# Kernel optimization log

Hardware: AMD Instinct MI355X
Metric: run time of the kernel (lower is better)

Reference implementation:

```python
import jax, jax.numpy as jnp
import numpy as np

HID = 128
K = 8
G = 1024        # number of graphs (jets)
N_SV = 16       # secondary vertices per graph
N_TRK = 64      # tracks per graph


def _mlp2(x, W1, b1, W2, b2):
    # Linear -> ELU -> Linear -> ReLU (the sv/trk encoders)
    h = jax.nn.elu(x @ W1 + b1)
    return jax.nn.relu(h @ W2 + b2)


def _dynamic_edge_conv(src, dst, W, b, k):
    # DynamicEdgeConv with bipartite input (x_src, x_dst):
    #   edge_index = knn(src, dst, k) per graph (Euclidean in feature space)
    #   message    = nn(cat([x_i, x_j - x_i]))  with x_i = dst(target), x_j = src(neighbor)
    #   aggr       = max over the k neighbors of each target
    # src: [G, Ns, D], dst: [G, Nq, D]
    dots = jnp.einsum('gqd,gsd->gqs', dst, src)
    d2 = (jnp.sum(dst * dst, -1)[:, :, None] - 2.0 * dots
          + jnp.sum(src * src, -1)[:, None, :])            # [G, Nq, Ns]
    _, idx = jax.lax.top_k(-d2, k)                          # k nearest sources, [G, Nq, k]
    xj = jax.vmap(lambda s, i: s[i])(src, idx)              # gather neighbors [G, Nq, k, D]
    xi = dst[:, :, None, :]                                 # [G, Nq, 1, D]
    edge_feat = jnp.concatenate([jnp.broadcast_to(xi, xj.shape), xj - xi], axis=-1)
    msg = jax.nn.elu(edge_feat @ W + b)                     # [G, Nq, k, D]
    return jnp.max(msg, axis=2)                             # max-scatter -> [G, Nq, D]


def setup_inputs() -> dict:
    key = jax.random.key(0)
    ks = jax.random.split(key, 16)
    s = 0.05
    inp = {
        'x_sv': jax.random.normal(ks[0], (G * N_SV, 2), jnp.float32),
        'x_trk': jax.random.normal(ks[1], (G * N_TRK, 8), jnp.float32),
        # sv encoder
        'W_sv1': jax.random.normal(ks[2], (2, HID), jnp.float32) * s,
        'b_sv1': jnp.zeros((HID,), jnp.float32),
        'W_sv2': jax.random.normal(ks[3], (HID, HID), jnp.float32) * s,
        'b_sv2': jnp.zeros((HID,), jnp.float32),
        # trk encoder
        'W_trk1': jax.random.normal(ks[4], (8, HID), jnp.float32) * s,
        'b_trk1': jnp.zeros((HID,), jnp.float32),
        'W_trk2': jax.random.normal(ks[5], (HID, HID), jnp.float32) * s,
        'b_trk2': jnp.zeros((HID,), jnp.float32),
        # edge-conv MLPs (Linear(2*HID, HID) + ELU)
        'W_c1': jax.random.normal(ks[6], (2 * HID, HID), jnp.float32) * s,
        'b_c1': jnp.zeros((HID,), jnp.float32),
        'W_c2': jax.random.normal(ks[7], (2 * HID, HID), jnp.float32) * s,
        'b_c2': jnp.zeros((HID,), jnp.float32),
        # output head 128->64->32->4->1
        'W_o1': jax.random.normal(ks[8], (HID, 64), jnp.float32) * s,
        'b_o1': jnp.zeros((64,), jnp.float32),
        'W_o2': jax.random.normal(ks[9], (64, 32), jnp.float32) * s,
        'b_o2': jnp.zeros((32,), jnp.float32),
        'W_o3': jax.random.normal(ks[10], (32, 4), jnp.float32) * s,
        'b_o3': jnp.zeros((4,), jnp.float32),
        'W_o4': jax.random.normal(ks[11], (4, 1), jnp.float32) * s,
        'b_o4': jnp.zeros((1,), jnp.float32),
        # block-structured batch assignment (sorted, equal-size graphs)
        'batch_sv': jnp.arange(G * N_SV, dtype=jnp.int64 if jax.config.jax_enable_x64 else jnp.int32) // N_SV,
        'batch_trk': jnp.arange(G * N_TRK, dtype=jnp.int64 if jax.config.jax_enable_x64 else jnp.int32) // N_TRK,
    }
    return inp


def reference(x_sv, x_trk, W_sv1, b_sv1, W_sv2, b_sv2, W_trk1, b_trk1, W_trk2, b_trk2,
              W_c1, b_c1, W_c2, b_c2, W_o1, b_o1, W_o2, b_o2, W_o3, b_o3, W_o4, b_o4,
              batch_sv, batch_trk):
    # Batches are equal-size contiguous blocks (see setup_inputs), so per-graph
    # knn/gather/max are expressed as batched ops over a leading G dimension.
    sv = _mlp2(x_sv, W_sv1, b_sv1, W_sv2, b_sv2).reshape(G, N_SV, HID)
    trk = _mlp2(x_trk, W_trk1, b_trk1, W_trk2, b_trk2).reshape(G, N_TRK, HID)
    # conv_1: sources = encoded SVs, targets = encoded tracks
    f1 = _dynamic_edge_conv(sv, trk, W_c1, b_c1, K)          # [G, N_TRK, HID]
    # conv_2: sources = f1 (per-track), targets = encoded tracks
    f2 = _dynamic_edge_conv(f1, trk, W_c2, b_c2, K)          # [G, N_TRK, HID]
    # avg_pool_x with cluster == batch: mean over tracks of each graph
    pooled = jnp.mean(f2, axis=1)                            # [G, HID]
    h = jax.nn.elu(pooled @ W_o1 + b_o1)
    h = jax.nn.elu(h @ W_o2 + b_o2)
    h = jax.nn.elu(h @ W_o3 + b_o3)
    out = h @ W_o4 + b_o4                                    # [G, 1]
    batch = jnp.arange(G)
    return out, batch
```

## Files before the change

kernel.cpp:

```cpp
#include <hip/hip_runtime.h>

#define G_    1024
#define TPB   512
#define INF_F 3.4e38f

typedef __attribute__((ext_vector_type(8))) short short8;
typedef __attribute__((ext_vector_type(4))) float f32x4;

__device__ __forceinline__ float elu_fast(float x) { return x > 0.f ? x : __expf(x) - 1.f; }
__device__ __forceinline__ float elu_ref(float x)  { return x > 0.f ? x : expm1f(x); }

#define RB(r, c)     ((r)*128 + (((c) + 8*(r)) & 127))

#define FMA4(acc_, sc_, wv_) do { (acc_).x = fmaf((sc_),(wv_).x,(acc_).x); \
                                  (acc_).y = fmaf((sc_),(wv_).y,(acc_).y); \
                                  (acc_).z = fmaf((sc_),(wv_).z,(acc_).z); \
                                  (acc_).w = fmaf((sc_),(wv_).w,(acc_).w); } while(0)
#define MAX4(mm_, bb_)       do { (mm_).x = fmaxf((mm_).x,(bb_).x); \
                                  (mm_).y = fmaxf((mm_).y,(bb_).y); \
                                  (mm_).z = fmaxf((mm_).z,(bb_).z); \
                                  (mm_).w = fmaxf((mm_).w,(bb_).w); } while(0)

#define MFMA1(acc_, A_, B_) \
    acc_ = __builtin_amdgcn_mfma_f32_16x16x32_bf16((A_), (B_), (acc_), 0, 0, 0)

__device__ __forceinline__ unsigned short bf16_of(float v) {
    unsigned u = __float_as_uint(v);
    u = u + 0x7FFFu + ((u >> 16) & 1u);
    return (unsigned short)(u >> 16);
}
__device__ __forceinline__ float f32_of(unsigned short h) {
    return __uint_as_float((unsigned)h << 16);
}

__global__ void prep_pack(const float* __restrict__ Wtrk2, const float* __restrict__ Wsv2,
                          const float* __restrict__ Wc1,   const float* __restrict__ Wc2,
                          unsigned short* __restrict__ wsu) {
    const int o = blockIdx.x * 256 + threadIdx.x;
    if (o >= 6 * 16384) return;
    const int m = o >> 14, pos = o & 16383;
    const int j = pos & 7, lane = (pos >> 3) & 63, tile = pos >> 9;
    const int ks = tile >> 3, ni = tile & 7;
    const int d = ks * 32 + (lane >> 4) * 8 + j;
    const int c = ni * 16 + (lane & 15);
    const int e = d * 128 + c;
    float v;
    switch (m) {
        case 0: v = Wtrk2[e]; break;
        case 1: v = Wsv2[e]; break;
        case 2: v = Wc1[16384 + e]; break;
        case 3: v = Wc1[e] - Wc1[16384 + e]; break;
        case 4: v = Wc2[e] - Wc2[16384 + e]; break;
        default: v = Wc2[16384 + e]; break;
    }
    wsu[m * 16384 + pos] = bf16_of(v);
}

#define LOADB1(B_, m_, pos_) B_ = *(const short8*)(wsu + (m_) * 16384 + (pos_))
#define LDFRAG(buf_, r_, k0_) (*(const short8*)&(buf_)[RB((r_), (k0_))])

__global__ __launch_bounds__(TPB, 8)
void fused_mfma(const float* __restrict__ x_sv,  const float* __restrict__ x_trk,
                const float* __restrict__ W_sv1, const float* __restrict__ b_sv1,
                const float* __restrict__ b_sv2,
                const float* __restrict__ W_trk1,const float* __restrict__ b_trk1,
                const float* __restrict__ b_trk2,
                const float* __restrict__ b_c1,  const float* __restrict__ b_c2,
                const float* __restrict__ W_o1,  const float* __restrict__ b_o1,
                const float* __restrict__ W_o2,  const float* __restrict__ b_o2,
                const float* __restrict__ W_o3,  const float* __restrict__ b_o3,
                const float* __restrict__ W_o4,  const float* __restrict__ b_o4,
                const unsigned short* __restrict__ wsu,
                float* __restrict__ out)
{
    __shared__ __align__(16) char sAraw[16384];
    __shared__ __align__(16) char sBraw[16384];
    __shared__ __align__(16) char sCraw[8192];
    short*    sAh = (short*)sAraw;    float* sAf = (float*)sAraw;
    short*    sBh = (short*)sBraw;    float* sBf = (float*)sBraw;
    unsigned* sBu = (unsigned*)sBraw;
    short*    sCh = (short*)sCraw;    float* sCf = (float*)sCraw;
    unsigned* sCu = (unsigned*)sCraw;

    const int g    = blockIdx.x;
    const int tid  = threadIdx.x;
    const int c128 = tid & 127;
    const int g4   = tid >> 7;
    const int wv   = tid >> 6;
    const int lane = tid & 63;
    const int quad = lane >> 4;
    const int ln   = lane & 15;

    sCf[tid] = x_trk[(size_t)g * 512 + tid];
    if (tid < 32) sCf[512 + tid] = x_sv[(size_t)g * 32 + tid];
    __syncthreads();

    {
        float w[8];
        #pragma unroll
        for (int k = 0; k < 8; k++) w[k] = W_trk1[k * 128 + c128];
        const float b1 = b_trk1[c128];
        #pragma unroll
        for (int i = 0; i < 16; i++) {
            const int r = g4 * 16 + i;
            float xr[8];
            *(float4*)&xr[0] = *(const float4*)&sCf[r * 8];
            *(float4*)&xr[4] = *(const float4*)&sCf[r * 8 + 4];
            float acc = b1;
            #pragma unroll
            for (int k = 0; k < 8; k++) acc = fmaf(xr[k], w[k], acc);
            sBh[RB(r, c128)] = bf16_of(elu_fast(acc));
        }
    }
    __syncthreads();

    {
        const int mi = wv >> 1, nb = (wv & 1) * 4;
        const int row = mi * 16 + ln;
        f32x4 acc[4];
        #pragma unroll
        for (int t = 0; t < 4; t++) {
            const float bz = b_trk2[(nb + t) * 16 + ln];
            acc[t] = (f32x4){bz, bz, bz, bz};
        }
        #pragma unroll 2
        for (int ks = 0; ks < 4; ks++) {
            const int k0 = ks * 32 + quad * 8;
            const short8 A = LDFRAG(sBh, row, k0);
            #pragma unroll
            for (int t = 0; t < 4; t++) {
                const int pos = ((ks * 8 + (nb + t)) * 64 + lane) * 8;
                short8 B;
                LOADB1(B, 0, pos);
                MFMA1(acc[t], A, B);
            }
        }
        #pragma unroll
        for (int t = 0; t < 4; t++)
            #pragma unroll
            for (int r = 0; r < 4; r++)
                sAh[RB(mi * 16 + quad * 4 + r, (nb + t) * 16 + ln)] =
                    bf16_of(fmaxf(acc[t][r], 0.f));
    }
    __syncthreads();

    {
        const float w0 = W_sv1[c128], w1 = W_sv1[128 + c128];
        const float b1 = b_sv1[c128];
        #pragma unroll
        for (int i = 0; i < 4; i++) {
            const int s = g4 * 4 + i;
            sBh[RB(s, c128)] = bf16_of(
                elu_fast(fmaf(sCf[512 + s * 2 + 1], w1, fmaf(sCf[512 + s * 2], w0, b1))));
        }
    }
    __syncthreads();

    {
        const int ni = wv;
        const float bz = b_sv2[ni * 16 + ln];
        f32x4 acc = (f32x4){bz, bz, bz, bz};
        #pragma unroll 2
        for (int ks = 0; ks < 4; ks++) {
            const int k0 = ks * 32 + quad * 8;
            const short8 A = LDFRAG(sBh, ln, k0);
            const int pos = ((ks * 8 + ni) * 64 + lane) * 8;
            short8 B;
            LOADB1(B, 1, pos);
            MFMA1(acc, A, B);
        }
        #pragma unroll
        for (int r = 0; r < 4; r++) {
            const float v = fmaxf(acc[r], 0.f);
            sCh[RB(quad * 4 + r, ni * 16 + ln)] = bf16_of(v);
            float p = v * v;
            #pragma unroll
            for (int o = 1; o <= 8; o <<= 1) p += __shfl_xor(p, o, 16);
            if (ln == 0) sBf[2048 + ni * 16 + quad * 4 + r] = p;
        }
    }
    __syncthreads();

    {
        const int ni = wv;
        const bool doP4 = (wv < 4);
        f32x4 accB = (f32x4){0.f, 0.f, 0.f, 0.f};
        f32x4 accS = (f32x4){0.f, 0.f, 0.f, 0.f};
        #pragma unroll 2
        for (int ks = 0; ks < 4; ks++) {
            const int k0 = ks * 32 + quad * 8;
            const short8 S = LDFRAG(sCh, ln, k0);
            const int pos = ((ks * 8 + ni) * 64 + lane) * 8;
            short8 B;
            LOADB1(B, 2, pos);
            MFMA1(accB, S, B);
            if (doP4) {
                const short8 T = LDFRAG(sAh, wv * 16 + ln, k0);
                MFMA1(accS, T, S);
            }
        }
        float nsv = 0.f;
        if (doP4) {
            #pragma unroll
            for (int p = 0; p < 8; p++) nsv += sBf[2048 + p * 16 + ln];
        }
        __syncthreads();
        #pragma unroll
        for (int r = 0; r < 4; r++)
            sCf[(quad * 4 + r) * 128 + ni * 16 + ln] = accB[r];
        if (doP4) {
            #pragma unroll
            for (int r = 0; r < 4; r++)
                sBf[(wv * 16 + quad * 4 + r) * 17 + ln] = fmaf(-2.f, accS[r], nsv);
        }
    }
    __syncthreads();

    {
        const int q  = tid >> 3;
        const int s0 = tid & 7;
        float sc0 = sBf[q * 17 + s0];
        float sc1 = sBf[q * 17 + s0 + 8];
        unsigned pack1 = 0u;
        #pragma unroll
        for (int r = 0; r < 8; r++) {
            float bv = sc0; int bs = s0;
            if (sc1 < bv) { bv = sc1; bs = s0 + 8; }
            #pragma unroll
            for (int o = 1; o <= 4; o <<= 1) {
                const float ov = __shfl_xor(bv, o, 8);
                const int   os = __shfl_xor(bs, o, 8);
                if (ov < bv || (ov == bv && os < bs)) { bv = ov; bs = os; }
            }
            pack1 |= (unsigned)bs << (4 * r);
            if (bs == s0)     sc0 = INF_F;
            if (bs == s0 + 8) sc1 = INF_F;
        }
        if (s0 == 0) sBu[1088 + q] = pack1;
    }
    __syncthreads();

    {
        const int mi = wv >> 1, nb = (wv & 1) * 4;
        const int row = mi * 16 + ln;
        f32x4 a1acc[4];
        #pragma unroll
        for (int t = 0; t < 4; t++) {
            const float bz1 = b_c1[(nb + t) * 16 + ln];
            a1acc[t] = (f32x4){bz1, bz1, bz1, bz1};
        }
        #pragma unroll 2
        for (int ks = 0; ks < 4; ks++) {
            const int k0 = ks * 32 + quad * 8;
            const short8 A = LDFRAG(sAh, row, k0);
            #pragma unroll
            for (int t = 0; t < 4; t++) {
                const int pos = ((ks * 8 + (nb + t)) * 64 + lane) * 8;
                short8 B;
                LOADB1(B, 3, pos);
                MFMA1(a1acc[t], A, B);
            }
        }
        unsigned pk[4];
        #pragma unroll
        for (int r = 0; r < 4; r++) pk[r] = sBu[1088 + mi * 16 + quad * 4 + r];
        __syncthreads();
        float np[4] = {0.f, 0.f, 0.f, 0.f};
        const int ccb = nb * 16 + ln;
        const float* b1base = &sCf[ccb];
        #pragma unroll
        for (int r = 0; r < 4; r++) {
            float mx0 = -INF_F, mx1 = -INF_F, mx2 = -INF_F, mx3 = -INF_F;
            #pragma unroll
            for (int j = 0; j < 8; j++) {
                const int s = (int)((pk[r] >> (4 * j)) & 15u);
                const float* rp = b1base + s * 128;
                mx0 = fmaxf(mx0, rp[0]);
                mx1 = fmaxf(mx1, rp[16]);
                mx2 = fmaxf(mx2, rp[32]);
                mx3 = fmaxf(mx3, rp[48]);
            }
            const float mxa[4] = {mx0, mx1, mx2, mx3};
            #pragma unroll
            for (int t = 0; t < 4; t++) {
                const float f = elu_fast(a1acc[t][r] + mxa[t]);
                sBh[RB(mi * 16 + quad * 4 + r, ccb + 16 * t)] = bf16_of(f);
                np[r] = fmaf(f, f, np[r]);
            }
        }
        #pragma unroll
        for (int r = 0; r < 4; r++) {
            #pragma unroll
            for (int o = 1; o <= 8; o <<= 1) np[r] += __shfl_xor(np[r], o, 16);
        }
        __syncthreads();
        if (ln == 0) {
            #pragma unroll
            for (int r = 0; r < 4; r++)
                sCf[(wv & 1) * 64 + mi * 16 + quad * 4 + r] = np[r];
        }
    }

    unsigned a2p[8];
    {
        const int mi = wv >> 1, nb = (wv & 1) * 4;
        const int row = mi * 16 + ln;
        f32x4 a2acc[4];
        #pragma unroll
        for (int t = 0; t < 4; t++) {
            const float bz2 = b_c2[(nb + t) * 16 + ln];
            a2acc[t] = (f32x4){bz2, bz2, bz2, bz2};
        }
        #pragma unroll 2
        for (int ks = 0; ks < 4; ks++) {
            const int k0 = ks * 32 + quad * 8;
            const short8 A = LDFRAG(sAh, row, k0);
            #pragma unroll
            for (int t = 0; t < 4; t++) {
                const int pos = ((ks * 8 + (nb + t)) * 64 + lane) * 8;
                short8 B;
                LOADB1(B, 4, pos);
                MFMA1(a2acc[t], A, B);
            }
        }
        #pragma unroll
        for (int t = 0; t < 4; t++) {
            a2p[2 * t]     = (unsigned)bf16_of(a2acc[t][0]) |
                             ((unsigned)bf16_of(a2acc[t][1]) << 16);
            a2p[2 * t + 1] = (unsigned)bf16_of(a2acc[t][2]) |
                             ((unsigned)bf16_of(a2acc[t][3]) << 16);
        }
    }
    __syncthreads();

    {
        const int mi = wv >> 1, nia = (wv & 1) * 2;
        const int row = mi * 16 + ln;
        float ns[2];
        #pragma unroll
        for (int u = 0; u < 2; u++) {
            const int s = (nia + u) * 16 + ln;
            ns[u] = sCf[s] + sCf[64 + s];
        }
        f32x4 acc[2];
        acc[0] = (f32x4){0.f, 0.f, 0.f, 0.f};
        acc[1] = (f32x4){0.f, 0.f, 0.f, 0.f};
        #pragma unroll 2
        for (int ks = 0; ks < 4; ks++) {
            const int k0 = ks * 32 + quad * 8;
            const short8 A = LDFRAG(sAh, row, k0);
            #pragma unroll
            for (int u = 0; u < 2; u++) {
                const short8 Bf = LDFRAG(sBh, (nia + u) * 16 + ln, k0);
                MFMA1(acc[u], A, Bf);
            }
        }
        __syncthreads();
        #pragma unroll
        for (int u = 0; u < 2; u++) {
            const int s = (nia + u) * 16 + ln;
            #pragma unroll
            for (int r = 0; r < 4; r++)
                sAf[(mi * 16 + quad * 4 + r) * 64 + s] = fmaf(-2.f, acc[u][r], ns[u]);
        }
    }
    __syncthreads();

    {
        const int q = tid >> 3;
        const int j = tid & 7;
        float v[8];
        *(float4*)&v[0] = *(const float4*)&sAf[q * 64 + 8 * j];
        *(float4*)&v[4] = *(const float4*)&sAf[q * 64 + 8 * j + 4];
        unsigned lo2 = 0u, hi2 = 0u;
        #pragma unroll
        for (int r = 0; r < 8; r++) {
            float bv = v[0]; int bs = 8 * j;
            #pragma unroll
            for (int t = 1; t < 8; t++)
                if (v[t] < bv) { bv = v[t]; bs = 8 * j + t; }
            #pragma unroll
            for (int o = 1; o <= 4; o <<= 1) {
                const float ov = __shfl_xor(bv, o, 8);
                const int   os = __shfl_xor(bs, o, 8);
                if (ov < bv || (ov == bv && os < bs)) { bv = ov; bs = os; }
            }
            if (r < 4) lo2 |= (unsigned)bs << (8 * r);
            else       hi2 |= (unsigned)bs << (8 * (r - 4));
            #pragma unroll
            for (int t = 0; t < 8; t++)
                if (bs == 8 * j + t) v[t] = INF_F;
        }
        if (j == 0) {
            sCu[128 + 2 * q]     = lo2;
            sCu[128 + 2 * q + 1] = hi2;
        }
    }
    __syncthreads();

    {
        const int mi = wv >> 1, nb = (wv & 1) * 4;
        const int row = mi * 16 + ln;
        f32x4 acc[4];
        #pragma unroll
        for (int t = 0; t < 4; t++) acc[t] = (f32x4){0.f, 0.f, 0.f, 0.f};
        #pragma unroll 2
        for (int ks = 0; ks < 4; ks++) {
            const int k0 = ks * 32 + quad * 8;
            const short8 A = LDFRAG(sBh, row, k0);
            #pragma unroll
            for (int t = 0; t < 4; t++) {
                const int pos = ((ks * 8 + (nb + t)) * 64 + lane) * 8;
                short8 B;
                LOADB1(B, 5, pos);
                MFMA1(acc[t], A, B);
            }
        }
        __syncthreads();
        float* bp = (mi < 2) ? sAf : sBf;
        const int ccb = nb * 16 + ln;
        #pragma unroll
        for (int t = 0; t < 4; t++)
            #pragma unroll
            for (int r = 0; r < 4; r++) {
                const int rr = mi * 16 + quad * 4 + r;
                bp[(rr & 31) * 128 + ccb + 16 * t] = acc[t][r];
            }
    }
    __syncthreads();

    {
        const int mi = wv >> 1, nb = (wv & 1) * 4;
        float ps[4] = {0.f, 0.f, 0.f, 0.f};
        const int ccb = nb * 16 + ln;
        const float* bA = &sAf[ccb];
        const float* bB = &sBf[ccb];
        #pragma unroll
        for (int r = 0; r < 4; r++) {
            const int rr = mi * 16 + quad * 4 + r;
            const unsigned plo = sCu[128 + 2 * rr];
            const unsigned phi = sCu[128 + 2 * rr + 1];
            float mx0 = -INF_F, mx1 = -INF_F, mx2 = -INF_F, mx3 = -INF_F;
            #pragma unroll
            for (int j = 0; j < 8; j++) {
                const int s = (int)(((j < 4) ? (plo >> (8 * j))
                                             : (phi >> (8 * (j - 4)))) & 63u);
                const float* rp = ((s < 32) ? bA : bB) + (s & 31) * 128;
                mx0 = fmaxf(mx0, rp[0]);
                mx1 = fmaxf(mx1, rp[16]);
                mx2 = fmaxf(mx2, rp[32]);
                mx3 = fmaxf(mx3, rp[48]);
            }
            const float mxa[4] = {mx0, mx1, mx2, mx3};
            #pragma unroll
            for (int t = 0; t < 4; t++) {
                const unsigned u = a2p[2 * t + (r >> 1)];
                const float a2v = __uint_as_float((r & 1) ? (u & 0xFFFF0000u) : (u << 16));
                ps[t] += elu_fast(a2v + mxa[t]);
            }
        }
        #pragma unroll
        for (int t = 0; t < 4; t++) {
            ps[t] += __shfl_xor(ps[t], 16, 64);
            ps[t] += __shfl_xor(ps[t], 32, 64);
        }
        __syncthreads();
        if (lane < 16)
            #pragma unroll
            for (int t = 0; t < 4; t++)
                sBf[mi * 128 + (nb + t) * 16 + lane] = ps[t];
    }
    __syncthreads();

    if (tid < 128) {
        const float p = (sBf[tid] + sBf[128 + tid] + sBf[256 + tid] + sBf[384 + tid]) * (1.f / 64.f);
        sBf[512 + tid] = p;
    }
    __syncthreads();
    if (tid < 64) {
        float acc = b_o1[tid];
        for (int d = 0; d < 128; d++) acc = fmaf(sBf[512 + d], W_o1[d * 64 + tid], acc);
        sBf[640 + tid] = elu_fast(acc);
    }
    __syncthreads();
    if (tid < 32) {
        float acc = b_o2[tid];
        for (int d = 0; d < 64; d++) acc = fmaf(sBf[640 + d], W_o2[d * 32 + tid], acc);
        sBf[704 + tid] = elu_fast(acc);
    }
    __syncthreads();
    if (tid < 4) {
        float acc = b_o3[tid];
        for (int d = 0; d < 32; d++) acc = fmaf(sBf[704 + d], W_o3[d * 4 + tid], acc);
        sBf[736 + tid] = elu_fast(acc);
    }
    __syncthreads();
    if (tid == 0) {
        float acc = b_o4[0];
        #pragma unroll
        for (int d = 0; d < 4; d++) acc = fmaf(sBf[736 + d], W_o4[d], acc);
        out[g] = acc;
        out[G_ + g] = (float)g;
    }
}

#define ROTV(r, d)    ((r)*128 + (((d) + 4*(r)) & 127))
#define BS1V(s, c)    (2048 + (s)*128 + (((c) + 4*(s)) & 127))
__global__ __launch_bounds__(TPB, 2)
void fused_vec(const float* __restrict__ x_sv,  const float* __restrict__ x_trk,
               const float* __restrict__ W_sv1, const float* __restrict__ b_sv1,
               const float* __restrict__ W_sv2, const float* __restrict__ b_sv2,
               const float* __restrict__ W_trk1,const float* __restrict__ b_trk1,
               const float* __restrict__ W_trk2,const float* __restrict__ b_trk2,
               const float* __restrict__ W_c1,  const float* __restrict__ b_c1,
               const float* __restrict__ W_c2,  const float* __restrict__ b_c2,
               const float* __restrict__ W_o1,  const float* __restrict__ b_o1,
               const float* __restrict__ W_o2,  const float* __restrict__ b_o2,
               const float* __restrict__ W_o3,  const float* __restrict__ b_o3,
               const float* __restrict__ W_o4,  const float* __restrict__ b_o4,
               float* __restrict__ out)
{
    __shared__ float sA[8192];
    __shared__ float sB[8192];
    __shared__ float sC[4096];
    const int g    = blockIdx.x;
    const int tid  = threadIdx.x;
    const int c128 = tid & 127;
    const int g4   = tid >> 7;
    const int cq   = tid & 31;
    const int c0   = cq * 4;
    const int rg   = tid >> 5;
    const int lane_hi = tid & 32;

    sC[2048 + tid] = x_trk[(size_t)g * 512 + tid];
    if (tid < 32) sC[2560 + tid] = x_sv[(size_t)g * 32 + tid];
    __syncthreads();
    {
        float w[8];
        #pragma unroll
        for (int k = 0; k < 8; k++) w[k] = W_trk1[k * 128 + c128];
        const float b1 = b_trk1[c128];
        #pragma unroll
        for (int i = 0; i < 16; i++) {
            const int r = g4 * 16 + i;
            float acc = b1;
            #pragma unroll
            for (int k = 0; k < 8; k++) acc = fmaf(sC[2048 + r * 8 + k], w[k], acc);
            sB[r * 128 + c128] = elu_ref(acc);
        }
    }
    __syncthreads();
    {
        const int r0 = rg * 4;
        float4 acc[4];
        const float4 bz = *(const float4*)&b_trk2[c0];
        #pragma unroll
        for (int i = 0; i < 4; i++) acc[i] = bz;
        for (int d0 = 0; d0 < 128; d0 += 4) {
            const float4 w0 = *(const float4*)&W_trk2[(d0 + 0) * 128 + c0];
            const float4 w1 = *(const float4*)&W_trk2[(d0 + 1) * 128 + c0];
            const float4 w2 = *(const float4*)&W_trk2[(d0 + 2) * 128 + c0];
            const float4 w3 = *(const float4*)&W_trk2[(d0 + 3) * 128 + c0];
            #pragma unroll
            for (int i = 0; i < 4; i++) {
                const float4 h = *(const float4*)&sB[(r0 + i) * 128 + d0];
                FMA4(acc[i], h.x, w0); FMA4(acc[i], h.y, w1);
                FMA4(acc[i], h.z, w2); FMA4(acc[i], h.w, w3);
            }
        }
        #pragma unroll
        for (int i = 0; i < 4; i++) {
            float4 r;
            r.x = fmaxf(acc[i].x, 0.f); r.y = fmaxf(acc[i].y, 0.f);
            r.z = fmaxf(acc[i].z, 0.f); r.w = fmaxf(acc[i].w, 0.f);
            *(float4*)&sA[ROTV(r0 + i, c0)] = r;
        }
    }
    __syncthreads();
    {
        const float w0 = W_sv1[c128], w1 = W_sv1[128 + c128];
        const float b1 = b_sv1[c128];
        #pragma unroll
        for (int i = 0; i < 4; i++) {
            const int s = g4 * 4 + i;
            sB[s * 128 + c128] =
                elu_ref(fmaf(sC[2560 + s * 2 + 1], w1, fmaf(sC[2560 + s * 2], w0, b1)));
        }
    }
    __syncthreads();
    {
        const int s = rg;
        float4 acc = *(const float4*)&b_sv2[c0];
        for (int d0 = 0; d0 < 128; d0 += 4) {
            const float4 w0 = *(const float4*)&W_sv2[(d0 + 0) * 128 + c0];
            const float4 w1 = *(const float4*)&W_sv2[(d0 + 1) * 128 + c0];
            const float4 w2 = *(const float4*)&W_sv2[(d0 + 2) * 128 + c0];
            const float4 w3 = *(const float4*)&W_sv2[(d0 + 3) * 128 + c0];
            const float4 h = *(const float4*)&sB[s * 128 + d0];
            FMA4(acc, h.x, w0); FMA4(acc, h.y, w1);
            FMA4(acc, h.z, w2); FMA4(acc, h.w, w3);
        }
        float4 r;
        r.x = fmaxf(acc.x, 0.f); r.y = fmaxf(acc.y, 0.f);
        r.z = fmaxf(acc.z, 0.f); r.w = fmaxf(acc.w, 0.f);
        *(float4*)&sC[ROTV(s, c0)] = r;
    }
    __syncthreads();
    unsigned pack1;
    {
        {
            const int s = rg;
            float4 acc = {0.f, 0.f, 0.f, 0.f};
            for (int d0 = 0; d0 < 128; d0 += 4) {
                const float4 e  = *(const float4*)&sC[ROTV(s, d0)];
                const float4 w0 = *(const float4*)&W_c1[(128 + d0 + 0) * 128 + c0];
                const float4 w1 = *(const float4*)&W_c1[(128 + d0 + 1) * 128 + c0];
                const float4 w2 = *(const float4*)&W_c1[(128 + d0 + 2) * 128 + c0];
                const float4 w3 = *(const float4*)&W_c1[(128 + d0 + 3) * 128 + c0];
                FMA4(acc, e.x, w0); FMA4(acc, e.y, w1);
                FMA4(acc, e.z, w2); FMA4(acc, e.w, w3);
            }
            *(float4*)&sC[BS1V(s, c0)] = acc;
        }
        const int q  = tid >> 3;
        const int s0 = tid & 7;
        float d0a = 0.f, d1a = 0.f, n0 = 0.f, n1 = 0.f;
        for (int d0 = 0; d0 < 128; d0 += 4) {
            const float4 t  = *(const float4*)&sA[ROTV(q, d0)];
            const float4 v0 = *(const float4*)&sC[ROTV(s0, d0)];
            const float4 v1 = *(const float4*)&sC[ROTV(s0 + 8, d0)];
            d0a += t.x * v0.x + t.y * v0.y + t.z * v0.z + t.w * v0.w;
            d1a += t.x * v1.x + t.y * v1.y + t.z * v1.z + t.w * v1.w;
            n0  += v0.x * v0.x + v0.y * v0.y + v0.z * v0.z + v0.w * v0.w;
            n1  += v1.x * v1.x + v1.y * v1.y + v1.z * v1.z + v1.w * v1.w;
        }
        float sc0 = fmaf(-2.f, d0a, n0);
        float sc1 = fmaf(-2.f, d1a, n1);
        pack1 = 0u;
        #pragma unroll
        for (int r = 0; r < 8; r++) {
            float bv = sc0; int bs = s0;
            if (sc1 < bv) { bv = sc1; bs = s0 + 8; }
            #pragma unroll
            for (int o = 1; o <= 4; o <<= 1) {
                const float ov = __shfl_xor(bv, o, 8);
                const int   os = __shfl_xor(bs, o, 8);
                if (ov < bv || (ov == bv && os < bs)) { bv = ov; bs = os; }
            }
            pack1 |= (unsigned)bs << (4 * r);
            if (bs == s0)     sc0 = INF_F;
            if (bs == s0 + 8) sc1 = INF_F;
        }
    }
    __syncthreads();
    float4 a2v[4];
    {
        const int q0 = rg * 4;
        float4 a1[4];
        const float4 bc1 = *(const float4*)&b_c1[c0];
        const float4 bc2 = *(const float4*)&b_c2[c0];
        #pragma unroll
        for (int i = 0; i < 4; i++) { a1[i] = bc1; a2v[i] = bc2; }
        for (int d0 = 0; d0 < 128; d0 += 4) {
            float4 t[4];
            #pragma unroll
            for (int i = 0; i < 4; i++) t[i] = *(const float4*)&sA[ROTV(q0 + i, d0)];
            #pragma unroll
            for (int dj = 0; dj < 4; dj++) {
                float4 wv;
                const float4 wa = *(const float4*)&W_c1[(d0 + dj) * 128 + c0];
                const float4 wb = *(const float4*)&W_c1[(128 + d0 + dj) * 128 + c0];
                wv.x = wa.x - wb.x; wv.y = wa.y - wb.y;
                wv.z = wa.z - wb.z; wv.w = wa.w - wb.w;
                FMA4(a1[0], ((const float*)&t[0])[dj], wv);
                FMA4(a1[1], ((const float*)&t[1])[dj], wv);
                FMA4(a1[2], ((const float*)&t[2])[dj], wv);
                FMA4(a1[3], ((const float*)&t[3])[dj], wv);
            }
            #pragma unroll
            for (int dj = 0; dj < 4; dj++) {
                float4 wv;
                const float4 wa = *(const float4*)&W_c2[(d0 + dj) * 128 + c0];
                const float4 wb = *(const float4*)&W_c2[(128 + d0 + dj) * 128 + c0];
                wv.x = wa.x - wb.x; wv.y = wa.y - wb.y;
                wv.z = wa.z - wb.z; wv.w = wa.w - wb.w;
                FMA4(a2v[0], ((const float*)&t[0])[dj], wv);
                FMA4(a2v[1], ((const float*)&t[1])[dj], wv);
                FMA4(a2v[2], ((const float*)&t[2])[dj], wv);
                FMA4(a2v[3], ((const float*)&t[3])[dj], wv);
            }
        }
        #pragma unroll
        for (int i = 0; i < 4; i++) {
            const int q = q0 + i;
            const unsigned pk = __shfl(pack1, 8 * i + lane_hi);
            float4 m = {-INF_F, -INF_F, -INF_F, -INF_F};
            #pragma unroll
            for (int j = 0; j < 8; j++) {
                const int s = (int)((pk >> (4 * j)) & 15u);
                const float4 b = *(const float4*)&sC[BS1V(s, c0)];
                MAX4(m, b);
            }
            float4 f;
            f.x = elu_ref(a1[i].x + m.x); f.y = elu_ref(a1[i].y + m.y);
            f.z = elu_ref(a1[i].z + m.z); f.w = elu_ref(a1[i].w + m.w);
            *(float4*)&sB[ROTV(q, c0)] = f;
        }
    }
    __syncthreads();
    {
        const int s  = tid & 63;
        const int q0 = (tid >> 6) * 8;
        float acc[8];
        #pragma unroll
        for (int i = 0; i < 8; i++) acc[i] = 0.f;
        float nrm = 0.f;
        for (int d0 = 0; d0 < 128; d0 += 4) {
            const float4 f = *(const float4*)&sB[ROTV(s, d0)];
            nrm = fmaf(f.x, f.x, nrm); nrm = fmaf(f.y, f.y, nrm);
            nrm = fmaf(f.z, f.z, nrm); nrm = fmaf(f.w, f.w, nrm);
            #pragma unroll
            for (int i = 0; i < 8; i++) {
                const float4 t = *(const float4*)&sA[ROTV(q0 + i, d0)];
                acc[i] = fmaf(t.x, f.x, acc[i]); acc[i] = fmaf(t.y, f.y, acc[i]);
                acc[i] = fmaf(t.z, f.z, acc[i]); acc[i] = fmaf(t.w, f.w, acc[i]);
            }
        }
        #pragma unroll
        for (int i = 0; i < 8; i++)
            sC[(q0 + i) * 64 + s] = fmaf(-2.f, acc[i], nrm);
    }
    __syncthreads();
    unsigned lo2, hi2;
    {
        const int q = tid >> 3;
        const int j = tid & 7;
        float v[8];
        *(float4*)&v[0] = *(const float4*)&sC[q * 64 + 8 * j];
        *(float4*)&v[4] = *(const float4*)&sC[q * 64 + 8 * j + 4];
        lo2 = 0u; hi2 = 0u;
        #pragma unroll
        for (int r = 0; r < 8; r++) {
            float bv = v[0]; int bs = 8 * j;
            #pragma unroll
            for (int t = 1; t < 8; t++)
                if (v[t] < bv) { bv = v[t]; bs = 8 * j + t; }
            #pragma unroll
            for (int o = 1; o <= 4; o <<= 1) {
                const float ov = __shfl_xor(bv, o, 8);
                const int   os = __shfl_xor(bs, o, 8);
                if (ov < bv || (ov == bv && os < bs)) { bv = ov; bs = os; }
            }
            if (r < 4) lo2 |= (unsigned)bs << (8 * r);
            else       hi2 |= (unsigned)bs << (8 * (r - 4));
            #pragma unroll
            for (int t = 0; t < 8; t++)
                if (bs == 8 * j + t) v[t] = INF_F;
        }
        const int r0 = rg * 4;
        float4 acc[4];
        #pragma unroll
        for (int i = 0; i < 4; i++) acc[i] = make_float4(0.f, 0.f, 0.f, 0.f);
        for (int d0 = 0; d0 < 128; d0 += 4) {
            const float4 w0 = *(const float4*)&W_c2[(128 + d0 + 0) * 128 + c0];
            const float4 w1 = *(const float4*)&W_c2[(128 + d0 + 1) * 128 + c0];
            const float4 w2 = *(const float4*)&W_c2[(128 + d0 + 2) * 128 + c0];
            const float4 w3 = *(const float4*)&W_c2[(128 + d0 + 3) * 128 + c0];
            #pragma unroll
            for (int i = 0; i < 4; i++) {
                const float4 f = *(const float4*)&sB[ROTV(r0 + i, d0)];
                FMA4(acc[i], f.x, w0); FMA4(acc[i], f.y, w1);
                FMA4(acc[i], f.z, w2); FMA4(acc[i], f.w, w3);
            }
        }
        #pragma unroll
        for (int i = 0; i < 4; i++)
            *(float4*)&sA[ROTV(r0 + i, c0)] = acc[i];
    }
    __syncthreads();
    {
        const int q0 = rg * 4;
        float4 ps = {0.f, 0.f, 0.f, 0.f};
        #pragma unroll
        for (int i = 0; i < 4; i++) {
            const unsigned plo = __shfl(lo2, 8 * i + lane_hi);
            const unsigned phi = __shfl(hi2, 8 * i + lane_hi);
            float4 m = {-INF_F, -INF_F, -INF_F, -INF_F};
            #pragma unroll
            for (int j = 0; j < 8; j++) {
                const int s = (int)(((j < 4) ? (plo >> (8 * j)) : (phi >> (8 * (j - 4)))) & 63u);
                const float4 b = *(const float4*)&sA[ROTV(s, c0)];
                MAX4(m, b);
            }
            ps.x += elu_ref(a2v[i].x + m.x); ps.y += elu_ref(a2v[i].y + m.y);
            ps.z += elu_ref(a2v[i].z + m.z); ps.w += elu_ref(a2v[i].w + m.w);
        }
        *(float4*)&sB[rg * 128 + c0] = ps;
    }
    __syncthreads();
    if (tid < 128) {
        float p = 0.f;
        #pragma unroll
        for (int t = 0; t < 16; t++) p += sB[t * 128 + tid];
        sB[2048 + tid] = p * (1.f / 64.f);
    }
    __syncthreads();
    if (tid < 64) {
        float acc = b_o1[tid];
        for (int d = 0; d < 128; d++) acc = fmaf(sB[2048 + d], W_o1[d * 64 + tid], acc);
        sB[2176 + tid] = elu_ref(acc);
    }
    __syncthreads();
    if (tid < 32) {
        float acc = b_o2[tid];
        for (int d = 0; d < 64; d++) acc = fmaf(sB[2176 + d], W_o2[d * 32 + tid], acc);
        sB[2240 + tid] = elu_ref(acc);
    }
    __syncthreads();
    if (tid < 4) {
        float acc = b_o3[tid];
        for (int d = 0; d < 32; d++) acc = fmaf(sB[2240 + d], W_o3[d * 4 + tid], acc);
        sB[2272 + tid] = elu_ref(acc);
    }
    __syncthreads();
    if (tid == 0) {
        float acc = b_o4[0];
        #pragma unroll
        for (int d = 0; d < 4; d++) acc = fmaf(sB[2272 + d], W_o4[d], acc);
        out[g] = acc;
        out[G_ + g] = (float)g;
    }
}

extern "C" void kernel_launch(void* const* d_in, const int* in_sizes, int n_in,
                              void* d_out, int out_size, void* d_ws, size_t ws_size,
                              hipStream_t stream) {
    const float* x_sv   = (const float*)d_in[0];
    const float* x_trk  = (const float*)d_in[1];
    const float* W_sv1  = (const float*)d_in[2];
    const float* b_sv1  = (const float*)d_in[3];
    const float* W_sv2  = (const float*)d_in[4];
    const float* b_sv2  = (const float*)d_in[5];
    const float* W_trk1 = (const float*)d_in[6];
    const float* b_trk1 = (const float*)d_in[7];
    const float* W_trk2 = (const float*)d_in[8];
    const float* b_trk2 = (const float*)d_in[9];
    const float* W_c1   = (const float*)d_in[10];
    const float* b_c1   = (const float*)d_in[11];
    const float* W_c2   = (const float*)d_in[12];
    const float* b_c2   = (const float*)d_in[13];
    const float* W_o1   = (const float*)d_in[14];
    const float* b_o1   = (const float*)d_in[15];
    const float* W_o2   = (const float*)d_in[16];
    const float* b_o2   = (const float*)d_in[17];
    const float* W_o3   = (const float*)d_in[18];
    const float* b_o3   = (const float*)d_in[19];
    const float* W_o4   = (const float*)d_in[20];
    const float* b_o4   = (const float*)d_in[21];
    float* out = (float*)d_out;

    const size_t WS_NEED = (size_t)6 * 16384 * sizeof(unsigned short);
    if (ws_size >= WS_NEED && d_ws != nullptr) {
        unsigned short* wsu = (unsigned short*)d_ws;
        prep_pack<<<384, 256, 0, stream>>>(W_trk2, W_sv2, W_c1, W_c2, wsu);
        fused_mfma<<<G_, TPB, 0, stream>>>(x_sv, x_trk, W_sv1, b_sv1, b_sv2,
                                           W_trk1, b_trk1, b_trk2, b_c1, b_c2,
                                           W_o1, b_o1, W_o2, b_o2, W_o3, b_o3,
                                           W_o4, b_o4, wsu, out);
    } else {
        fused_vec<<<G_, TPB, 0, stream>>>(x_sv, x_trk, W_sv1, b_sv1, W_sv2, b_sv2,
                                          W_trk1, b_trk1, W_trk2, b_trk2,
                                          W_c1, b_c1, W_c2, b_c2,
                                          W_o1, b_o1, W_o2, b_o2, W_o3, b_o3,
                                          W_o4, b_o4, out);
    }
}
```

Baseline: 167.9 us.

## Restructure MFMA stages to cut live accumulators and remap final gather per column

```diff
diff --git a/kernel.cpp b/kernel.cpp
--- a/kernel.cpp
+++ b/kernel.cpp
@@ -31,6 +31,9 @@
 }
 __device__ __forceinline__ float f32_of(unsigned short h) {
     return __uint_as_float((unsigned)h << 16);
+}
+__device__ __forceinline__ unsigned packbf2(float a, float b) {
+    return (unsigned)bf16_of(a) | ((unsigned)bf16_of(b) << 16);
 }
 
 __global__ void prep_pack(const float* __restrict__ Wtrk2, const float* __restrict__ Wsv2,
@@ -80,7 +83,6 @@
     short*    sBh = (short*)sBraw;    float* sBf = (float*)sBraw;
     unsigned* sBu = (unsigned*)sBraw;
     short*    sCh = (short*)sCraw;    float* sCf = (float*)sCraw;
-    unsigned* sCu = (unsigned*)sCraw;
 
     const int g    = blockIdx.x;
     const int tid  = threadIdx.x;
@@ -115,32 +117,28 @@
     __syncthreads();
 
     {
-        const int mi = wv >> 1, nb = (wv & 1) * 4;
-        const int row = mi * 16 + ln;
-        f32x4 acc[4];
-        #pragma unroll
-        for (int t = 0; t < 4; t++) {
-            const float bz = b_trk2[(nb + t) * 16 + ln];
-            acc[t] = (f32x4){bz, bz, bz, bz};
-        }
-        #pragma unroll 2
-        for (int ks = 0; ks < 4; ks++) {
-            const int k0 = ks * 32 + quad * 8;
-            const short8 A = LDFRAG(sBh, row, k0);
-            #pragma unroll
-            for (int t = 0; t < 4; t++) {
-                const int pos = ((ks * 8 + (nb + t)) * 64 + lane) * 8;
+        const int cb = wv * 16 + ln;
+        const float bz = b_trk2[cb];
+        #pragma unroll 1
+        for (int half = 0; half < 2; half++) {
+            f32x4 a0 = (f32x4){bz, bz, bz, bz};
+            f32x4 a1 = (f32x4){bz, bz, bz, bz};
+            #pragma unroll 2
+            for (int ks = 0; ks < 4; ks++) {
+                const int k0 = ks * 32 + quad * 8;
+                const short8 A0 = LDFRAG(sBh, half * 32 + ln, k0);
+                const short8 A1 = LDFRAG(sBh, half * 32 + 16 + ln, k0);
                 short8 B;
-                LOADB1(B, 0, pos);
-                MFMA1(acc[t], A, B);
-            }
-        }
-        #pragma unroll
-        for (int t = 0; t < 4; t++)
-            #pragma unroll
-            for (int r = 0; r < 4; r++)
-                sAh[RB(mi * 16 + quad * 4 + r, (nb + t) * 16 + ln)] =
-                    bf16_of(fmaxf(acc[t][r], 0.f));
+                LOADB1(B, 0, ((ks * 8 + wv) * 64 + lane) * 8);
+                MFMA1(a0, A0, B);
+                MFMA1(a1, A1, B);
+            }
+            #pragma unroll
+            for (int r = 0; r < 4; r++) {
+                sAh[RB(half * 32 + quad * 4 + r, cb)]      = bf16_of(fmaxf(a0[r], 0.f));
+                sAh[RB(half * 32 + 16 + quad * 4 + r, cb)] = bf16_of(fmaxf(a1[r], 0.f));
+            }
+        }
     }
     __syncthreads();
 
@@ -164,9 +162,8 @@
         for (int ks = 0; ks < 4; ks++) {
             const int k0 = ks * 32 + quad * 8;
             const short8 A = LDFRAG(sBh, ln, k0);
-            const int pos = ((ks * 8 + ni) * 64 + lane) * 8;
             short8 B;
-            LOADB1(B, 1, pos);
+            LOADB1(B, 1, ((ks * 8 + ni) * 64 + lane) * 8);
             MFMA1(acc, A, B);
         }
         #pragma unroll
@@ -190,9 +187,8 @@
         for (int ks = 0; ks < 4; ks++) {
             const int k0 = ks * 32 + quad * 8;
             const short8 S = LDFRAG(sCh, ln, k0);
-            const int pos = ((ks * 8 + ni) * 64 + lane) * 8;
             short8 B;
-            LOADB1(B, 2, pos);
+            LOADB1(B, 2, ((ks * 8 + ni) * 64 + lane) * 8);
             MFMA1(accB, S, B);
             if (doP4) {
                 const short8 T = LDFRAG(sAh, wv * 16 + ln, k0);
@@ -243,49 +239,47 @@
     {
         const int mi = wv >> 1, nb = (wv & 1) * 4;
         const int row = mi * 16 + ln;
-        f32x4 a1acc[4];
-        #pragma unroll
-        for (int t = 0; t < 4; t++) {
-            const float bz1 = b_c1[(nb + t) * 16 + ln];
-            a1acc[t] = (f32x4){bz1, bz1, bz1, bz1};
-        }
-        #pragma unroll 2
-        for (int ks = 0; ks < 4; ks++) {
-            const int k0 = ks * 32 + quad * 8;
-            const short8 A = LDFRAG(sAh, row, k0);
-            #pragma unroll
-            for (int t = 0; t < 4; t++) {
-                const int pos = ((ks * 8 + (nb + t)) * 64 + lane) * 8;
-                short8 B;
-                LOADB1(B, 3, pos);
-                MFMA1(a1acc[t], A, B);
-            }
-        }
+        const int ccb = nb * 16 + ln;
         unsigned pk[4];
         #pragma unroll
         for (int r = 0; r < 4; r++) pk[r] = sBu[1088 + mi * 16 + quad * 4 + r];
-        __syncthreads();
         float np[4] = {0.f, 0.f, 0.f, 0.f};
-        const int ccb = nb * 16 + ln;
-        const float* b1base = &sCf[ccb];
-        #pragma unroll
-        for (int r = 0; r < 4; r++) {
-            float mx0 = -INF_F, mx1 = -INF_F, mx2 = -INF_F, mx3 = -INF_F;
-            #pragma unroll
-            for (int j = 0; j < 8; j++) {
-                const int s = (int)((pk[r] >> (4 * j)) & 15u);
-                const float* rp = b1base + s * 128;
-                mx0 = fmaxf(mx0, rp[0]);
-                mx1 = fmaxf(mx1, rp[16]);
-                mx2 = fmaxf(mx2, rp[32]);
-                mx3 = fmaxf(mx3, rp[48]);
-            }
-            const float mxa[4] = {mx0, mx1, mx2, mx3};
-            #pragma unroll
-            for (int t = 0; t < 4; t++) {
-                const float f = elu_fast(a1acc[t][r] + mxa[t]);
-                sBh[RB(mi * 16 + quad * 4 + r, ccb + 16 * t)] = bf16_of(f);
-                np[r] = fmaf(f, f, np[r]);
+        #pragma unroll 1
+        for (int half = 0; half < 2; half++) {
+            f32x4 a0, a1c;
+            {
+                const float bz0 = b_c1[(nb + half * 2) * 16 + ln];
+                const float bz1 = b_c1[(nb + half * 2 + 1) * 16 + ln];
+                a0  = (f32x4){bz0, bz0, bz0, bz0};
+                a1c = (f32x4){bz1, bz1, bz1, bz1};
+            }
+            #pragma unroll 2
+            for (int ks = 0; ks < 4; ks++) {
+                const int k0 = ks * 32 + quad * 8;
+                const short8 A = LDFRAG(sAh, row, k0);
+                short8 B0, B1;
+                LOADB1(B0, 3, ((ks * 8 + nb + half * 2) * 64 + lane) * 8);
+                LOADB1(B1, 3, ((ks * 8 + nb + half * 2 + 1) * 64 + lane) * 8);
+                MFMA1(a0, A, B0);
+                MFMA1(a1c, A, B1);
+            }
+            if (half == 0) __syncthreads();
+            #pragma unroll
+            for (int r = 0; r < 4; r++) {
+                float mx0 = -INF_F, mx1 = -INF_F;
+                #pragma unroll
+                for (int j = 0; j < 8; j++) {
+                    const int s = (int)((pk[r] >> (4 * j)) & 15u);
+                    const float* rp = &sCf[s * 128 + ccb + half * 32];
+                    mx0 = fmaxf(mx0, rp[0]);
+                    mx1 = fmaxf(mx1, rp[16]);
+                }
+                const float f0 = elu_fast(a0[r] + mx0);
+                const float f1v = elu_fast(a1c[r] + mx1);
+                sBh[RB(mi * 16 + quad * 4 + r, ccb + half * 32)]      = bf16_of(f0);
+                sBh[RB(mi * 16 + quad * 4 + r, ccb + half * 32 + 16)] = bf16_of(f1v);
+                np[r] = fmaf(f0, f0, np[r]);
+                np[r] = fmaf(f1v, f1v, np[r]);
             }
         }
         #pragma unroll
@@ -303,32 +297,26 @@
 
     unsigned a2p[8];
     {
-        const int mi = wv >> 1, nb = (wv & 1) * 4;
-        const int row = mi * 16 + ln;
-        f32x4 a2acc[4];
-        #pragma unroll
-        for (int t = 0; t < 4; t++) {
-            const float bz2 = b_c2[(nb + t) * 16 + ln];
-            a2acc[t] = (f32x4){bz2, bz2, bz2, bz2};
-        }
-        #pragma unroll 2
-        for (int ks = 0; ks < 4; ks++) {
-            const int k0 = ks * 32 + quad * 8;
-            const short8 A = LDFRAG(sAh, row, k0);
-            #pragma unroll
-            for (int t = 0; t < 4; t++) {
-                const int pos = ((ks * 8 + (nb + t)) * 64 + lane) * 8;
+        const int cb = wv * 16 + ln;
+        const float bz2 = b_c2[cb];
+        #pragma unroll 1
+        for (int half = 0; half < 2; half++) {
+            f32x4 a0 = (f32x4){bz2, bz2, bz2, bz2};
+            f32x4 a1 = (f32x4){bz2, bz2, bz2, bz2};
+            #pragma unroll 2
+            for (int ks = 0; ks < 4; ks++) {
+                const int k0 = ks * 32 + quad * 8;
+                const short8 A0 = LDFRAG(sAh, half * 32 + ln, k0);
+                const short8 A1 = LDFRAG(sAh, half * 32 + 16 + ln, k0);
                 short8 B;
-                LOADB1(B, 4, pos);
-                MFMA1(a2acc[t], A, B);
-            }
-        }
-        #pragma unroll
-        for (int t = 0; t < 4; t++) {
-            a2p[2 * t]     = (unsigned)bf16_of(a2acc[t][0]) |
-                             ((unsigned)bf16_of(a2acc[t][1]) << 16);
-            a2p[2 * t + 1] = (unsigned)bf16_of(a2acc[t][2]) |
-                             ((unsigned)bf16_of(a2acc[t][3]) << 16);
+                LOADB1(B, 4, ((ks * 8 + wv) * 64 + lane) * 8);
+                MFMA1(a0, A0, B);
+                MFMA1(a1, A1, B);
+            }
+            a2p[half * 4 + 0] = packbf2(a0[0], a0[1]);
+            a2p[half * 4 + 1] = packbf2(a0[2], a0[3]);
+            a2p[half * 4 + 2] = packbf2(a1[0], a1[1]);
+            a2p[half * 4 + 3] = packbf2(a1[2], a1[3]);
         }
     }
     __syncthreads();
@@ -366,13 +354,14 @@
     }
     __syncthreads();
 
+    unsigned lo2, hi2;
     {
         const int q = tid >> 3;
         const int j = tid & 7;
         float v[8];
         *(float4*)&v[0] = *(const float4*)&sAf[q * 64 + 8 * j];
         *(float4*)&v[4] = *(const float4*)&sAf[q * 64 + 8 * j + 4];
-        unsigned lo2 = 0u, hi2 = 0u;
+        lo2 = 0u; hi2 = 0u;
         #pragma unroll
         for (int r = 0; r < 8; r++) {
             float bv = v[0]; int bs = 8 * j;
@@ -391,114 +380,118 @@
             for (int t = 0; t < 8; t++)
                 if (bs == 8 * j + t) v[t] = INF_F;
         }
-        if (j == 0) {
-            sCu[128 + 2 * q]     = lo2;
-            sCu[128 + 2 * q + 1] = hi2;
-        }
-    }
-    __syncthreads();
-
-    {
-        const int mi = wv >> 1, nb = (wv & 1) * 4;
-        const int row = mi * 16 + ln;
-        f32x4 acc[4];
-        #pragma unroll
-        for (int t = 0; t < 4; t++) acc[t] = (f32x4){0.f, 0.f, 0.f, 0.f};
+    }
+    __syncthreads();
+
+    {
+        const int cb = wv * 16 + ln;
+        {
+            f32x4 a0 = (f32x4){0.f, 0.f, 0.f, 0.f};
+            f32x4 a1 = (f32x4){0.f, 0.f, 0.f, 0.f};
+            #pragma unroll 2
+            for (int ks = 0; ks < 4; ks++) {
+                const int k0 = ks * 32 + quad * 8;
+                const short8 A0 = LDFRAG(sBh, ln, k0);
+                const short8 A1 = LDFRAG(sBh, 16 + ln, k0);
+                short8 B;
+                LOADB1(B, 5, ((ks * 8 + wv) * 64 + lane) * 8);
+                MFMA1(a0, A0, B);
+                MFMA1(a1, A1, B);
+            }
+            #pragma unroll
+            for (int r = 0; r < 4; r++) {
+                sAf[(quad * 4 + r) * 128 + cb]        = a0[r];
+                sAf[(16 + quad * 4 + r) * 128 + cb]   = a1[r];
+            }
+        }
+        {
+            f32x4 a = (f32x4){0.f, 0.f, 0.f, 0.f};
+            #pragma unroll 2
+            for (int ks = 0; ks < 4; ks++) {
+                const int k0 = ks * 32 + quad * 8;
+                const short8 A = LDFRAG(sBh, 32 + ln, k0);
+                short8 B;
+                LOADB1(B, 5, ((ks * 8 + wv) * 64 + lane) * 8);
+                MFMA1(a, A, B);
+            }
+            #pragma unroll
+            for (int r = 0; r < 4; r++)
+                sCf[(quad * 4 + r) * 128 + cb] = a[r];
+        }
+        f32x4 c = (f32x4){0.f, 0.f, 0.f, 0.f};
         #pragma unroll 2
         for (int ks = 0; ks < 4; ks++) {
             const int k0 = ks * 32 + quad * 8;
-            const short8 A = LDFRAG(sBh, row, k0);
-            #pragma unroll
-            for (int t = 0; t < 4; t++) {
-                const int pos = ((ks * 8 + (nb + t)) * 64 + lane) * 8;
-                short8 B;
-                LOADB1(B, 5, pos);
-                MFMA1(acc[t], A, B);
-            }
+            const short8 A = LDFRAG(sBh, 48 + ln, k0);
+            short8 B;
+            LOADB1(B, 5, ((ks * 8 + wv) * 64 + lane) * 8);
+            MFMA1(c, A, B);
         }
         __syncthreads();
-        float* bp = (mi < 2) ? sAf : sBf;
-        const int ccb = nb * 16 + ln;
-        #pragma unroll
-        for (int t = 0; t < 4; t++)
+        #pragma unroll
+        for (int r = 0; r < 4; r++)
+            sBf[(quad * 4 + r) * 128 + cb] = c[r];
+        if ((tid & 7) == 0) {
+            const int q = tid >> 3;
+            sBu[2048 + 2 * q] = lo2;
+            sBu[2049 + 2 * q] = hi2;
+        }
+    }
+    __syncthreads();
+
+    {
+        const int cb = wv * 16 + ln;
+        float ps = 0.f;
+        #pragma unroll
+        for (int k = 0; k < 4; k++) {
             #pragma unroll
             for (int r = 0; r < 4; r++) {
-                const int rr = mi * 16 + quad * 4 + r;
-                bp[(rr & 31) * 128 + ccb + 16 * t] = acc[t][r];
-            }
-    }
-    __syncthreads();
-
-    {
-        const int mi = wv >> 1, nb = (wv & 1) * 4;
-        float ps[4] = {0.f, 0.f, 0.f, 0.f};
-        const int ccb = nb * 16 + ln;
-        const float* bA = &sAf[ccb];
-        const float* bB = &sBf[ccb];
-        #pragma unroll
-        for (int r = 0; r < 4; r++) {
-            const int rr = mi * 16 + quad * 4 + r;
-            const unsigned plo = sCu[128 + 2 * rr];
-            const unsigned phi = sCu[128 + 2 * rr + 1];
-            float mx0 = -INF_F, mx1 = -INF_F, mx2 = -INF_F, mx3 = -INF_F;
-            #pragma unroll
-            for (int j = 0; j < 8; j++) {
-                const int s = (int)(((j < 4) ? (plo >> (8 * j))
-                                             : (phi >> (8 * (j - 4)))) & 63u);
-                const float* rp = ((s < 32) ? bA : bB) + (s & 31) * 128;
-                mx0 = fmaxf(mx0, rp[0]);
-                mx1 = fmaxf(mx1, rp[16]);
-                mx2 = fmaxf(mx2, rp[32]);
-                mx3 = fmaxf(mx3, rp[48]);
-            }
-            const float mxa[4] = {mx0, mx1, mx2, mx3};
-            #pragma unroll
-            for (int t = 0; t < 4; t++) {
-                const unsigned u = a2p[2 * t + (r >> 1)];
+                const int rr = k * 16 + quad * 4 + r;
+                const unsigned plo = sBu[2048 + 2 * rr];
+                const unsigned phi = sBu[2049 + 2 * rr];
+                float mx = -INF_F;
+                #pragma unroll
+                for (int j = 0; j < 8; j++) {
+                    const int s = (int)(((j < 4) ? (plo >> (8 * j))
+                                                 : (phi >> (8 * (j - 4)))) & 63u);
+                    const float* rp = (s < 32) ? &sAf[s * 128]
+                                    : (s < 48) ? &sCf[(s - 32) * 128]
+                                               : &sBf[(s - 48) * 128];
+                    mx = fmaxf(mx, rp[cb]);
+                }
+                const unsigned u = a2p[k * 2 + (r >> 1)];
                 const float a2v = __uint_as_float((r & 1) ? (u & 0xFFFF0000u) : (u << 16));
-                ps[t] += elu_fast(a2v + mxa[t]);
-            }
-        }
-        #pragma unroll
-        for (int t = 0; t < 4; t++) {
-            ps[t] += __shfl_xor(ps[t], 16, 64);
-            ps[t] += __shfl_xor(ps[t], 32, 64);
-        }
-        __syncthreads();
-        if (lane < 16)
-            #pragma unroll
-            for (int t = 0; t < 4; t++)
-                sBf[mi * 128 + (nb + t) * 16 + lane] = ps[t];
-    }
-    __syncthreads();
-
-    if (tid < 128) {
-        const float p = (sBf[tid] + sBf[128 + tid] + sBf[256 + tid] + sBf[384 + tid]) * (1.f / 64.f);
-        sBf[512 + tid] = p;
-    }
-    __syncthreads();
+                ps += elu_fast(a2v + mx);
+            }
+        }
+        ps += __shfl_xor(ps, 16, 64);
+        ps += __shfl_xor(ps, 32, 64);
+        if (lane < 16) sBf[2560 + wv * 16 + lane] = ps * (1.f / 64.f);
+    }
+    __syncthreads();
+
     if (tid < 64) {
         float acc = b_o1[tid];
-        for (int d = 0; d < 128; d++) acc = fmaf(sBf[512 + d], W_o1[d * 64 + tid], acc);
-        sBf[640 + tid] = elu_fast(acc);
+        for (int d = 0; d < 128; d++) acc = fmaf(sBf[2560 + d], W_o1[d * 64 + tid], acc);
+        sBf[2688 + tid] = elu_fast(acc);
     }
     __syncthreads();
     if (tid < 32) {
         float acc = b_o2[tid];
-        for (int d = 0; d < 64; d++) acc = fmaf(sBf[640 + d], W_o2[d * 32 + tid], acc);
-        sBf[704 + tid] = elu_fast(acc);
+        for (int d = 0; d < 64; d++) acc = fmaf(sBf[2688 + d], W_o2[d * 32 + tid], acc);
+        sBf[2752 + tid] = elu_fast(acc);
     }
     __syncthreads();
     if (tid < 4) {
         float acc = b_o3[tid];
-        for (int d = 0; d < 32; d++) acc = fmaf(sBf[704 + d], W_o3[d * 4 + tid], acc);
-        sBf[736 + tid] = elu_fast(acc);
+        for (int d = 0; d < 32; d++) acc = fmaf(sBf[2752 + d], W_o3[d * 4 + tid], acc);
+        sBf[2784 + tid] = elu_fast(acc);
     }
     __syncthreads();
     if (tid == 0) {
         float acc = b_o4[0];
         #pragma unroll
-        for (int d = 0; d < 4; d++) acc = fmaf(sBf[736 + d], W_o4[d], acc);
+        for (int d = 0; d < 4; d++) acc = fmaf(sBf[2784 + d], W_o4[d], acc);
         out[g] = acc;
         out[G_ + g] = (float)g;
     }
```

After: 215.6 us. 1.28x slower.
